# Performance work log

Measured on AMD Instinct MI355X. Metric: run time of the kernel, lower is better.

## Reference

```python
import jax, jax.numpy as jnp
import numpy as np

KS = 3
PAD = 1
N = KS * KS  # 9 sampling points per output location


def setup_inputs() -> dict:
    key = jax.random.key(0)
    k1, k2, k3 = jax.random.split(key, 3)
    b, c, H, W, outc = 4, 128, 64, 64, 128
    x = jax.random.normal(k1, (b, c, H, W), jnp.float32)
    offset = jax.random.normal(k2, (b, 2 * N, H, W), jnp.float32)
    weight = jax.random.normal(k3, (outc, c, KS, KS), jnp.float32) * 0.05
    return {"x": x, "offset": offset, "weight": weight}


def reference(x, offset, weight):
    b, c, H, W = x.shape
    h, w = offset.shape[2], offset.shape[3]
    # reorder interleaved (x,y,x,y,...) offset channels to (all x, all y)
    idx = jnp.concatenate([jnp.arange(0, 2 * N, 2), jnp.arange(1, 2 * N, 2)])
    offset = offset[:, idx]
    # zero padding
    xp = jnp.pad(x, ((0, 0), (0, 0), (PAD, PAD), (PAD, PAD)))
    Hp, Wp = H + 2 * PAD, W + 2 * PAD
    # kernel-relative offsets p_n: [1, 2N, 1, 1]
    r = np.arange(-(KS - 1) // 2, (KS - 1) // 2 + 1)
    pnx, pny = np.meshgrid(r, r, indexing='ij')
    p_n = jnp.asarray(np.concatenate([pnx.flatten(), pny.flatten()]).reshape(1, 2 * N, 1, 1), jnp.float32)
    # base grid p_0: [1, 2N, h, w], coords start at 1 (padded frame)
    p0x, p0y = np.meshgrid(np.arange(1, h + 1), np.arange(1, w + 1), indexing='ij')
    p_0 = jnp.asarray(np.concatenate([np.tile(p0x.reshape(1, 1, h, w), (1, N, 1, 1)),
                                      np.tile(p0y.reshape(1, 1, h, w), (1, N, 1, 1))], axis=1), jnp.float32)
    p = jnp.transpose(p_0 + p_n + offset, (0, 2, 3, 1))  # [b, h, w, 2N]
    px, py = p[..., :N], p[..., N:]
    fx, fy = jnp.floor(px), jnp.floor(py)
    # 4 corner integer coords, clamped to padded image
    q_lt_x = jnp.clip(fx, 0, Hp - 1).astype(jnp.int32)
    q_lt_y = jnp.clip(fy, 0, Wp - 1).astype(jnp.int32)
    q_rb_x = jnp.clip(fx + 1, 0, Hp - 1).astype(jnp.int32)
    q_rb_y = jnp.clip(fy + 1, 0, Wp - 1).astype(jnp.int32)
    # out-of-range mask: snap p to floor(p) there (matches original, incl. zero grad thru floor)
    mask_x = jax.lax.stop_gradient(((px < PAD) | (px > Hp - 1 - PAD)).astype(px.dtype))
    mask_y = jax.lax.stop_gradient(((py < PAD) | (py > Wp - 1 - PAD)).astype(py.dtype))
    px = px * (1 - mask_x) + fx * mask_x
    py = py * (1 - mask_y) + fy * mask_y
    px = jnp.clip(px, 0, Hp - 1)
    py = jnp.clip(py, 0, Wp - 1)
    qltx = q_lt_x.astype(px.dtype); qlty = q_lt_y.astype(px.dtype)
    qrbx = q_rb_x.astype(px.dtype); qrby = q_rb_y.astype(px.dtype)
    # bilinear weights: [b, h, w, N]
    g_lt = (1 + (qltx - px)) * (1 + (qlty - py))
    g_rb = (1 - (qrbx - px)) * (1 - (qrby - py))
    g_lb = (1 + (qltx - px)) * (1 - (qrby - py))
    g_rt = (1 - (qrbx - px)) * (1 + (qlty - py))

    xv = xp.reshape(b, c, Hp * Wp)

    def gather(qx, qy):
        lin = (qx * Wp + qy).reshape(b, 1, h * w * N)
        g = jnp.take_along_axis(xv, jnp.broadcast_to(lin, (b, c, h * w * N)), axis=2)
        return g.reshape(b, c, h, w, N)

    x_off = (g_lt[:, None] * gather(q_lt_x, q_lt_y)
             + g_rb[:, None] * gather(q_rb_x, q_rb_y)
             + g_lb[:, None] * gather(q_lt_x, q_rb_y)
             + g_rt[:, None] * gather(q_rb_x, q_lt_y))  # [b, c, h, w, N]
    # N = i*ks + j -> out[(h,i),(w,j)]
    xo = x_off.reshape(b, c, h, w, KS, KS).transpose(0, 1, 2, 4, 3, 5).reshape(b, c, h * KS, w * KS)
    out = jax.lax.conv_general_dilated(xo, weight, window_strides=(KS, KS), padding='VALID',
                                       dimension_numbers=('NCHW', 'OIHW', 'NCHW'))
    return out
```

## Files before the change

kernel.cpp:

```cpp
#include <hip/hip_runtime.h>


typedef __bf16  v8bf16 __attribute__((ext_vector_type(8)));
typedef __bf16  bf16x2 __attribute__((ext_vector_type(2)));
typedef float   f32x4  __attribute__((ext_vector_type(4)));
typedef unsigned short ushort4v __attribute__((ext_vector_type(4)));
typedef _Float16 half4v __attribute__((ext_vector_type(4)));

#define CIN  128
#define NPT  9
#define KTOT 1152
#define OC   128
#define PX   32
#define NDESC (NPT * PX)
#define KSTEPS 36
#define LDB  (KTOT + 8)

__global__ __launch_bounds__(256) void xpose_kernel(const float* __restrict__ x,
                                                    __bf16* __restrict__ xt) {
    __shared__ float tile[64][33];
    const int bidx = blockIdx.x;
    const int b   = bidx >> 8;
    const int hw0 = ((bidx >> 2) & 63) * 64;
    const int c0  = (bidx & 3) * 32;
    const int tid = threadIdx.x;
    #pragma unroll
    for (int r = 0; r < 8; ++r) {
        int c_l  = (tid >> 6) + r * 4;
        int hw_l = tid & 63;
        tile[hw_l][c_l] = x[((size_t)(b * CIN + c0 + c_l) << 12) + hw0 + hw_l];
    }
    __syncthreads();
    #pragma unroll
    for (int r = 0; r < 8; ++r) {
        int hw_l = (tid >> 5) + r * 8;
        int c_l  = tid & 31;
        xt[((size_t)(b * 4096 + hw0 + hw_l)) * CIN + c0 + c_l] = (__bf16)tile[hw_l][c_l];
    }
}

__global__ __launch_bounds__(256) void wfrag_kernel(const float* __restrict__ w,
                                                    __bf16* __restrict__ wfrag) {
    int t = blockIdx.x * 256 + threadIdx.x;
    if (t >= 8 * KSTEPS * 64) return;
    int lane = t & 63;
    int ks   = (t >> 6) % KSTEPS;
    int ot   = t / (KSTEPS * 64);
    int o    = ot * 16 + (lane & 15);
    v8bf16 frag;
    #pragma unroll
    for (int e = 0; e < 8; ++e) {
        int k   = ks * 32 + (lane >> 4) * 8 + e;
        int tap = k >> 7, c = k & 127;
        frag[e] = (__bf16)w[(size_t)o * KTOT + c * NPT + tap];
    }
    *(v8bf16*)(wfrag + (size_t)t * 8) = frag;
}

__global__ __launch_bounds__(512, 4) void deform_mfma_kernel(
    const float* __restrict__ x, const float* __restrict__ off,
    const float* __restrict__ w, const __bf16* __restrict__ wfrag,
    const __bf16* __restrict__ xt, float* __restrict__ out, int mode)
{
    __shared__ __align__(16) __bf16 Bt[PX][LDB];
    __shared__ __align__(8)  unsigned short sIdxP[NDESC][4];
    __shared__ __align__(8)  _Float16      sGP[NDESC][4];

    const int bidx = blockIdx.x;
    const int b   = bidx >> 7;
    const int i   = (bidx >> 1) & 63;
    const int j0  = (bidx & 1) * PX;
    const int tid = threadIdx.x;

    if (tid < NDESC) {
        int k = tid >> 5, p = tid & 31;
        int j = j0 + p;
        float ox = off[(((b * 18) + 2 * k) * 64 + i) * 64 + j];
        float oy = off[(((b * 18) + 2 * k + 1) * 64 + i) * 64 + j];
        float px = (float)(i + k / 3) + ox;
        float py = (float)(j + k % 3) + oy;
        float fx = floorf(px), fy = floorf(py);
        int qltx = (int)fminf(fmaxf(fx, 0.f), 65.f);
        int qlty = (int)fminf(fmaxf(fy, 0.f), 65.f);
        int qrbx = (int)fminf(fmaxf(fx + 1.f, 0.f), 65.f);
        int qrby = (int)fminf(fmaxf(fy + 1.f, 0.f), 65.f);
        if (px < 1.f || px > 64.f) px = fx;
        if (py < 1.f || py > 64.f) py = fy;
        px = fminf(fmaxf(px, 0.f), 65.f);
        py = fminf(fmaxf(py, 0.f), 65.f);
        float wxl = 1.f + (float)qltx - px;
        float wxr = 1.f - ((float)qrbx - px);
        float wyl = 1.f + (float)qlty - py;
        float wyr = 1.f - ((float)qrby - py);
        float g[4] = { wxl * wyl, wxr * wyr, wxl * wyr, wxr * wyl };
        int qx[4] = { qltx, qrbx, qltx, qrbx };
        int qy[4] = { qlty, qrby, qrby, qlty };
        #pragma unroll
        for (int cr = 0; cr < 4; ++cr) {
            bool inb = (qx[cr] >= 1) && (qx[cr] <= 64) && (qy[cr] >= 1) && (qy[cr] <= 64);
            sIdxP[tid][cr] = inb ? (unsigned short)((qx[cr] - 1) * 64 + (qy[cr] - 1)) : 0;
            sGP[tid][cr]   = inb ? (_Float16)g[cr] : (_Float16)0.f;
        }
    }
    __syncthreads();

    const int l  = tid & 63;
    const int wv = tid >> 6;

    if (mode == 2) {
        const __bf16* xtb = xt + ((size_t)b * 4096) * CIN;
        #pragma unroll 2
        for (int dd = 0; dd < NDESC / 8; ++dd) {
            int d = wv * (NDESC / 8) + dd;
            int tap = d >> 5, p = d & 31;
            ushort4v id = *(const ushort4v*)&sIdxP[d][0];
            half4v   gh = *(const half4v*)&sGP[d][0];
            float s0 = 0.f, s1 = 0.f;
            #pragma unroll
            for (int cr = 0; cr < 4; ++cr) {
                unsigned int v = *(const unsigned int*)(xtb + (size_t)id[cr] * CIN + 2 * l);
                float c0, c1;
                unsigned int lo = v << 16, hi = v & 0xffff0000u;
                __builtin_memcpy(&c0, &lo, 4);
                __builtin_memcpy(&c1, &hi, 4);
                float gf = (float)gh[cr];
                s0 += gf * c0;
                s1 += gf * c1;
            }
            bf16x2 pr = { (__bf16)s0, (__bf16)s1 };
            *(bf16x2*)&Bt[p][tap * CIN + 2 * l] = pr;
        }
    } else {
        const float* xb = x + ((size_t)b * CIN << 12);
        for (int dd = 0; dd < NDESC / 8; ++dd) {
            int d = wv * (NDESC / 8) + dd;
            int tap = d >> 5, p = d & 31;
            ushort4v id = *(const ushort4v*)&sIdxP[d][0];
            half4v   gh = *(const half4v*)&sGP[d][0];
            float s0 = 0.f, s1 = 0.f;
            #pragma unroll
            for (int cr = 0; cr < 4; ++cr) {
                float gf = (float)gh[cr];
                s0 += gf * xb[((size_t)(2 * l) << 12) + id[cr]];
                s1 += gf * xb[((size_t)(2 * l + 1) << 12) + id[cr]];
            }
            bf16x2 pr = { (__bf16)s0, (__bf16)s1 };
            *(bf16x2*)&Bt[p][tap * CIN + 2 * l] = pr;
        }
    }
    __syncthreads();

    const int ph   = wv >> 2;
    const int ob   = wv & 3;
    const int quad = l >> 4;
    const int lr   = l & 15;

    f32x4 acc0 = {0.f, 0.f, 0.f, 0.f};
    f32x4 acc1 = {0.f, 0.f, 0.f, 0.f};

    const __bf16* brow = &Bt[ph * 16 + lr][quad * 8];

    #pragma unroll 4
    for (int ks = 0; ks < KSTEPS; ++ks) {
        v8bf16 bfrag = *(const v8bf16*)(brow + ks * 32);
        #pragma unroll
        for (int mt = 0; mt < 2; ++mt) {
            int ot = ob * 2 + mt;
            v8bf16 afrag;
            if (mode >= 1) {
                afrag = *(const v8bf16*)(wfrag + (((size_t)ot * KSTEPS + ks) * 64 + l) * 8);
            } else {
                int o = ot * 16 + lr;
                #pragma unroll
                for (int e = 0; e < 8; ++e) {
                    int k = ks * 32 + quad * 8 + e;
                    int tap = k >> 7, c = k & 127;
                    afrag[e] = (__bf16)w[(size_t)o * KTOT + c * NPT + tap];
                }
            }
            if (mt == 0)
                acc0 = __builtin_amdgcn_mfma_f32_16x16x32_bf16(afrag, bfrag, acc0, 0, 0, 0);
            else
                acc1 = __builtin_amdgcn_mfma_f32_16x16x32_bf16(afrag, bfrag, acc1, 0, 0, 0);
        }
    }

    #pragma unroll
    for (int mt = 0; mt < 2; ++mt) {
        int obase = ob * 32 + mt * 16 + quad * 4;
        float* op = out + (((size_t)(b * OC + obase)) << 12) + (i << 6) + j0 + ph * 16 + lr;
        f32x4 a = (mt == 0) ? acc0 : acc1;
        #pragma unroll
        for (int r = 0; r < 4; ++r)
            op[(size_t)r << 12] = a[r];
    }
}

extern "C" void kernel_launch(void* const* d_in, const int* in_sizes, int n_in,
                              void* d_out, int out_size, void* d_ws, size_t ws_size,
                              hipStream_t stream) {
    const float* x   = (const float*)d_in[0];
    const float* off = (const float*)d_in[1];
    const float* w   = (const float*)d_in[2];
    float* out = (float*)d_out;

    const size_t wfrag_bytes = (size_t)OC * KTOT * sizeof(__bf16);
    const size_t xt_bytes    = (size_t)4 * 4096 * CIN * sizeof(__bf16);
    int mode = 0;
    if (ws_size >= wfrag_bytes + xt_bytes) mode = 2;
    else if (ws_size >= wfrag_bytes) mode = 1;

    __bf16* wfrag = (__bf16*)d_ws;
    __bf16* xt    = (__bf16*)((char*)d_ws + wfrag_bytes);

    if (mode >= 1) {
        wfrag_kernel<<<(8 * KSTEPS * 64 + 255) / 256, 256, 0, stream>>>(w, wfrag);
    }
    if (mode == 2) {
        xpose_kernel<<<4 * 64 * 4, 256, 0, stream>>>(x, xt);
    }
    deform_mfma_kernel<<<4 * 64 * 2, 512, 0, stream>>>(x, off, w, wfrag, xt, out, mode);
}
```

Measured before the change: 102.0 us.

## Chunk the deformable gather over tap groups to shrink LDS and raise occupancy

```diff
diff --git a/kernel.cpp b/kernel.cpp
--- a/kernel.cpp
+++ b/kernel.cpp
@@ -14,7 +14,9 @@
 #define PX   32
 #define NDESC (NPT * PX)
 #define KSTEPS 36
-#define LDB  (KTOT + 8)
+#define TAPG 3
+#define KSC  12
+#define LDBc 392
 
 __global__ __launch_bounds__(256) void xpose_kernel(const float* __restrict__ x,
                                                     __bf16* __restrict__ xt) {
@@ -57,12 +59,12 @@
     *(v8bf16*)(wfrag + (size_t)t * 8) = frag;
 }
 
-__global__ __launch_bounds__(512, 4) void deform_mfma_kernel(
+__global__ __launch_bounds__(512, 6) void deform_mfma_kernel(
     const float* __restrict__ x, const float* __restrict__ off,
     const float* __restrict__ w, const __bf16* __restrict__ wfrag,
     const __bf16* __restrict__ xt, float* __restrict__ out, int mode)
 {
-    __shared__ __align__(16) __bf16 Bt[PX][LDB];
+    __shared__ __align__(16) __bf16 Bt[PX][LDBc];
     __shared__ __align__(8)  unsigned short sIdxP[NDESC][4];
     __shared__ __align__(8)  _Float16      sGP[NDESC][4];
 
@@ -104,92 +106,91 @@
     }
     __syncthreads();
 
-    const int l  = tid & 63;
-    const int wv = tid >> 6;
-
-    if (mode == 2) {
-        const __bf16* xtb = xt + ((size_t)b * 4096) * CIN;
-        #pragma unroll 2
-        for (int dd = 0; dd < NDESC / 8; ++dd) {
-            int d = wv * (NDESC / 8) + dd;
-            int tap = d >> 5, p = d & 31;
-            ushort4v id = *(const ushort4v*)&sIdxP[d][0];
-            half4v   gh = *(const half4v*)&sGP[d][0];
-            float s0 = 0.f, s1 = 0.f;
-            #pragma unroll
-            for (int cr = 0; cr < 4; ++cr) {
-                unsigned int v = *(const unsigned int*)(xtb + (size_t)id[cr] * CIN + 2 * l);
-                float c0, c1;
-                unsigned int lo = v << 16, hi = v & 0xffff0000u;
-                __builtin_memcpy(&c0, &lo, 4);
-                __builtin_memcpy(&c1, &hi, 4);
-                float gf = (float)gh[cr];
-                s0 += gf * c0;
-                s1 += gf * c1;
-            }
-            bf16x2 pr = { (__bf16)s0, (__bf16)s1 };
-            *(bf16x2*)&Bt[p][tap * CIN + 2 * l] = pr;
-        }
-    } else {
-        const float* xb = x + ((size_t)b * CIN << 12);
-        for (int dd = 0; dd < NDESC / 8; ++dd) {
-            int d = wv * (NDESC / 8) + dd;
-            int tap = d >> 5, p = d & 31;
-            ushort4v id = *(const ushort4v*)&sIdxP[d][0];
-            half4v   gh = *(const half4v*)&sGP[d][0];
-            float s0 = 0.f, s1 = 0.f;
-            #pragma unroll
-            for (int cr = 0; cr < 4; ++cr) {
-                float gf = (float)gh[cr];
-                s0 += gf * xb[((size_t)(2 * l) << 12) + id[cr]];
-                s1 += gf * xb[((size_t)(2 * l + 1) << 12) + id[cr]];
-            }
-            bf16x2 pr = { (__bf16)s0, (__bf16)s1 };
-            *(bf16x2*)&Bt[p][tap * CIN + 2 * l] = pr;
-        }
-    }
-    __syncthreads();
-
-    const int ph   = wv >> 2;
-    const int ob   = wv & 3;
+    const int l    = tid & 63;
+    const int wv   = tid >> 6;
     const int quad = l >> 4;
     const int lr   = l & 15;
 
     f32x4 acc0 = {0.f, 0.f, 0.f, 0.f};
     f32x4 acc1 = {0.f, 0.f, 0.f, 0.f};
 
-    const __bf16* brow = &Bt[ph * 16 + lr][quad * 8];
-
-    #pragma unroll 4
-    for (int ks = 0; ks < KSTEPS; ++ks) {
-        v8bf16 bfrag = *(const v8bf16*)(brow + ks * 32);
-        #pragma unroll
-        for (int mt = 0; mt < 2; ++mt) {
-            int ot = ob * 2 + mt;
+    const __bf16* xtb = xt + ((size_t)b * 4096) * CIN;
+    const float*  xb  = x + ((size_t)b * CIN << 12);
+    const __bf16* brow0 = &Bt[lr][quad * 8];
+    const __bf16* brow1 = &Bt[16 + lr][quad * 8];
+
+    for (int t = 0; t < 3; ++t) {
+        if (mode == 2) {
+            #pragma unroll 4
+            for (int dd = 0; dd < KSC; ++dd) {
+                int dl = wv * KSC + dd;
+                int tap_l = dl >> 5, p = dl & 31;
+                int d = t * 96 + dl;
+                ushort4v id = *(const ushort4v*)&sIdxP[d][0];
+                half4v   gh = *(const half4v*)&sGP[d][0];
+                float s0 = 0.f, s1 = 0.f;
+                #pragma unroll
+                for (int cr = 0; cr < 4; ++cr) {
+                    unsigned int v = *(const unsigned int*)(xtb + (size_t)id[cr] * CIN + 2 * l);
+                    float c0v, c1v;
+                    unsigned int lo = v << 16, hi = v & 0xffff0000u;
+                    __builtin_memcpy(&c0v, &lo, 4);
+                    __builtin_memcpy(&c1v, &hi, 4);
+                    float gf = (float)gh[cr];
+                    s0 += gf * c0v;
+                    s1 += gf * c1v;
+                }
+                bf16x2 pr = { (__bf16)s0, (__bf16)s1 };
+                *(bf16x2*)&Bt[p][tap_l * CIN + 2 * l] = pr;
+            }
+        } else {
+            for (int dd = 0; dd < KSC; ++dd) {
+                int dl = wv * KSC + dd;
+                int tap_l = dl >> 5, p = dl & 31;
+                int d = t * 96 + dl;
+                ushort4v id = *(const ushort4v*)&sIdxP[d][0];
+                half4v   gh = *(const half4v*)&sGP[d][0];
+                float s0 = 0.f, s1 = 0.f;
+                #pragma unroll
+                for (int cr = 0; cr < 4; ++cr) {
+                    float gf = (float)gh[cr];
+                    s0 += gf * xb[((size_t)(2 * l) << 12) + id[cr]];
+                    s1 += gf * xb[((size_t)(2 * l + 1) << 12) + id[cr]];
+                }
+                bf16x2 pr = { (__bf16)s0, (__bf16)s1 };
+                *(bf16x2*)&Bt[p][tap_l * CIN + 2 * l] = pr;
+            }
+        }
+        __syncthreads();
+
+        #pragma unroll 4
+        for (int ks = 0; ks < KSC; ++ks) {
+            int ks_g = t * KSC + ks;
+            v8bf16 bfrag0 = *(const v8bf16*)(brow0 + ks * 32);
+            v8bf16 bfrag1 = *(const v8bf16*)(brow1 + ks * 32);
             v8bf16 afrag;
             if (mode >= 1) {
-                afrag = *(const v8bf16*)(wfrag + (((size_t)ot * KSTEPS + ks) * 64 + l) * 8);
+                afrag = *(const v8bf16*)(wfrag + (((size_t)wv * KSTEPS + ks_g) * 64 + l) * 8);
             } else {
-                int o = ot * 16 + lr;
+                int o = wv * 16 + lr;
                 #pragma unroll
                 for (int e = 0; e < 8; ++e) {
-                    int k = ks * 32 + quad * 8 + e;
+                    int k = ks_g * 32 + quad * 8 + e;
                     int tap = k >> 7, c = k & 127;
                     afrag[e] = (__bf16)w[(size_t)o * KTOT + c * NPT + tap];
                 }
             }
-            if (mt == 0)
-                acc0 = __builtin_amdgcn_mfma_f32_16x16x32_bf16(afrag, bfrag, acc0, 0, 0, 0);
-            else
-                acc1 = __builtin_amdgcn_mfma_f32_16x16x32_bf16(afrag, bfrag, acc1, 0, 0, 0);
+            acc0 = __builtin_amdgcn_mfma_f32_16x16x32_bf16(afrag, bfrag0, acc0, 0, 0, 0);
+            acc1 = __builtin_amdgcn_mfma_f32_16x16x32_bf16(afrag, bfrag1, acc1, 0, 0, 0);
         }
-    }
-
-    #pragma unroll
-    for (int mt = 0; mt < 2; ++mt) {
-        int obase = ob * 32 + mt * 16 + quad * 4;
+        if (t < 2) __syncthreads();
+    }
+
+    #pragma unroll
+    for (int ph = 0; ph < 2; ++ph) {
+        int obase = wv * 16 + quad * 4;
         float* op = out + (((size_t)(b * OC + obase)) << 12) + (i << 6) + j0 + ph * 16 + lr;
-        f32x4 a = (mt == 0) ? acc0 : acc1;
+        f32x4 a = (ph == 0) ? acc0 : acc1;
         #pragma unroll
         for (int r = 0; r < 4; ++r)
             op[(size_t)r << 12] = a[r];
```

Result: slower. 110.4 us (+8.3%).
